# Performance work log

Measured on AMD Instinct MI355X. Metric: run time of the kernel, lower is better.

The kernel has to match this reference:

```python
import jax, jax.numpy as jnp
import numpy as np

EPS = 1e-8
BOX2D_IDX = jnp.array([0, 1, 3, 4, 6])  # x, y, dx, dy, yaw


def box2corners(box):
    # box: (..., 5) = (x, y, w, h, alpha) -> corners (..., 4, 2), CCW order
    x, y, w, h, a = (box[..., i] for i in range(5))
    tx = jnp.array([0.5, -0.5, -0.5, 0.5], box.dtype)
    ty = jnp.array([0.5, 0.5, -0.5, -0.5], box.dtype)
    x4 = tx * w[..., None]
    y4 = ty * h[..., None]
    c, s = jnp.cos(a)[..., None], jnp.sin(a)[..., None]
    rx = c * x4 - s * y4 + x[..., None]
    ry = s * x4 + c * y4 + y[..., None]
    return jnp.stack([rx, ry], axis=-1)


def edge_intersections(c1, c2):
    # all 4x4 edge-edge intersections of two quads -> pts (..., 16, 2), mask (..., 16)
    p1 = c1[..., :, None, :]
    p2 = jnp.roll(c1, -1, axis=-2)[..., :, None, :]
    q1 = c2[..., None, :, :]
    q2 = jnp.roll(c2, -1, axis=-2)[..., None, :, :]
    r = p2 - p1
    s = q2 - q1
    denom = r[..., 0] * s[..., 1] - r[..., 1] * s[..., 0]
    safe = jnp.where(jnp.abs(denom) < EPS, 1.0, denom)
    qp = q1 - p1
    t = (qp[..., 0] * s[..., 1] - qp[..., 1] * s[..., 0]) / safe
    u = (qp[..., 0] * r[..., 1] - qp[..., 1] * r[..., 0]) / safe
    mask = (jnp.abs(denom) > EPS) & (t > 0) & (t < 1) & (u > 0) & (u < 1)
    pts = jnp.where(mask[..., None], p1 + t[..., None] * r, 0.0)
    lead = pts.shape[:-3]
    return pts.reshape(lead + (16, 2)), mask.reshape(lead + (16,))


def points_in_box(pts, corners):
    # pts (..., K, 2) inside rotated quad given by corners (..., 4, 2) -> (..., K) bool
    a = corners[..., 0:1, :]
    ab = corners[..., 1:2, :] - a
    ad = corners[..., 3:4, :] - a
    ap = pts - a
    pab = jnp.sum(ap * ab, -1)
    pad = jnp.sum(ap * ad, -1)
    nab = jnp.sum(ab * ab, -1)
    nad = jnp.sum(ad * ad, -1)
    return (pab > 0) & (pab < nab) & (pad > 0) & (pad < nad)


def masked_polygon_area(verts, mask):
    # verts (..., 24, 2) candidate vertices, mask (..., 24) validity
    m = mask.astype(verts.dtype)
    num = jnp.maximum(jnp.sum(m, -1, keepdims=True), 1.0)
    mean = jnp.sum(verts * m[..., None], -2, keepdims=True) / num[..., None]
    d = verts - mean  # centered (shoelace is translation-invariant)
    ang = jnp.arctan2(d[..., 1], d[..., 0])
    # push invalid vertices to the end with stable tie-break
    ang = jnp.where(mask, ang, 1e6 + jnp.arange(24, dtype=ang.dtype))
    idx = jnp.argsort(ang, axis=-1)
    vs = jnp.take_along_axis(d, idx[..., None], axis=-2)
    ms = jnp.take_along_axis(mask, idx, axis=-1)
    v0 = vs[..., 0:1, :]
    vs = jnp.where(ms[..., None], vs, v0)  # collapse invalid onto first vertex
    nxt = jnp.roll(vs, -1, axis=-2)
    cross = vs[..., 0] * nxt[..., 1] - vs[..., 1] * nxt[..., 0]
    return 0.5 * jnp.abs(jnp.sum(cross, -1))


def rotated_iou_3d(b1, b2):
    # b1, b2: (..., 7) = (x, y, z, dx, dy, dz, yaw); elementwise-aligned IoU
    c1 = box2corners(b1[..., BOX2D_IDX])
    c2 = box2corners(b2[..., BOX2D_IDX])
    ipts, imask = edge_intersections(c1, c2)
    in1 = points_in_box(c1, c2)
    in2 = points_in_box(c2, c1)
    verts = jnp.concatenate([c1, c2, ipts], axis=-2)  # (..., 24, 2)
    mask = jnp.concatenate([in1, in2, imask], axis=-1)
    inter2d = masked_polygon_area(verts, mask)
    zmax = jnp.minimum(b1[..., 2] + 0.5 * b1[..., 5], b2[..., 2] + 0.5 * b2[..., 5])
    zmin = jnp.maximum(b1[..., 2] - 0.5 * b1[..., 5], b2[..., 2] - 0.5 * b2[..., 5])
    inter3d = inter2d * jnp.maximum(zmax - zmin, 0.0)
    v1 = b1[..., 3] * b1[..., 4] * b1[..., 5]
    v2 = b2[..., 3] * b2[..., 4] * b2[..., 5]
    return inter3d / (v1 + v2 - inter3d + EPS)


def setup_inputs() -> dict:
    key = jax.random.key(0)
    k1, k2, k3, k4, k5 = jax.random.split(key, 5)
    N = 1048576
    ctr = (jax.random.uniform(k1, (N, 3)) - 0.5) * 40.0
    dims = jax.random.uniform(k2, (N, 3)) * 2.0 + 0.5
    yaw = (jax.random.uniform(k3, (N, 1)) - 0.5) * (2.0 * np.pi)
    pred = jnp.concatenate([ctr, dims, yaw], axis=-1).astype(jnp.float32)
    noise = jax.random.normal(k4, (N, 7)) * jnp.array(
        [0.3, 0.3, 0.3, 0.2, 0.2, 0.2, 0.2], jnp.float32)
    target = pred + noise
    target = target.at[:, 3:6].set(jnp.maximum(target[:, 3:6], 0.1))
    weight = jax.random.uniform(k5, (N,), dtype=jnp.float32)
    return {"pred": pred, "target": target, "weight": weight}


def reference(pred, target, weight):
    # IoU3DLoss(with_yaw=True, reduction='mean', loss_weight=1.0)
    loss_weight = 1.0
    iou = rotated_iou_3d(pred[None, ...], target[None, ...])  # (1, N)
    iou_loss = (1.0 - iou) * weight
    return loss_weight * jnp.mean(iou_loss)
```

## Files before the change

### kernel.cpp

```cpp
#include <hip/hip_runtime.h>

#define EPS_F 1e-8f

__device__ __forceinline__ float fast_rcp(float x) {
    return __builtin_amdgcn_rcpf(x);
}

__global__ void zero_out_kernel(float* out) { out[0] = 0.f; }

__device__ __forceinline__ float edge_contrib(float ax, float ay,
                                              float bx, float by,
                                              float W, float H) {
    float dx = bx - ax, dy = by - ay;
    float sdx = (fabsf(dx) < 1e-20f) ? 1e-20f : dx;
    float sdy = (fabsf(dy) < 1e-20f) ? 1e-20f : dy;
    float rdx = fast_rcp(sdx);
    float rdy = fast_rcp(sdy);

    float tA = (-W - ax) * rdx;
    float tB = ( W - ax) * rdx;
    float ta = fmaxf(fminf(tA, tB), 0.f);
    float tb = fminf(fmaxf(tA, tB), 1.f);
    tb = fmaxf(ta, tb);

    float u0 = (-H - ay) * rdy;
    float u1 = ( H - ay) * rdy;
    float tm0 = fminf(u0, u1), tm1 = fmaxf(u0, u1);
    float t1 = fminf(fmaxf(tm0, ta), tb);
    float t2 = fminf(fmaxf(tm1, ta), tb);

    float x0 = fmaf(ta, dx, ax), y0 = fmaf(ta, dy, ay);
    float x1 = fmaf(t1, dx, ax), y1 = fmaf(t1, dy, ay);
    float x2 = fmaf(t2, dx, ax), y2 = fmaf(t2, dy, ay);
    float x3 = fmaf(tb, dx, ax), y3 = fmaf(tb, dy, ay);
    float h0 = fminf(fmaxf(y0, -H), H) + H;
    float h1 = fminf(fmaxf(y1, -H), H) + H;
    float h2 = fminf(fmaxf(y2, -H), H) + H;
    float h3 = fminf(fmaxf(y3, -H), H) + H;

    return (x1 - x0) * (h0 + h1) + (x2 - x1) * (h1 + h2) + (x3 - x2) * (h2 + h3);
}

#define EPT 2

__global__ __launch_bounds__(256) void iou3d_loss_kernel(
    const float* __restrict__ pred, const float* __restrict__ target,
    const float* __restrict__ weight, float* __restrict__ out,
    int N, float invN)
{
    int base = blockIdx.x * (256 * EPT) + threadIdx.x;
    float val = 0.f;

    #pragma unroll
    for (int e = 0; e < EPT; ++e) {
        int i = base + e * 256;
        if (i >= N) continue;

        float b1[7], b2[7];
        #pragma unroll
        for (int k = 0; k < 7; ++k) b1[k] = pred[(long)i * 7 + k];
        #pragma unroll
        for (int k = 0; k < 7; ++k) b2[k] = target[(long)i * 7 + k];
        float wgt = weight[i];

        float s1, c1, s2, c2;
        __sincosf(b1[6], &s1, &c1);
        __sincosf(b2[6], &s2, &c2);
        float cd = c1 * c2 + s1 * s2;
        float sd = c1 * s2 - s1 * c2;
        float dxc = b2[0] - b1[0], dyc = b2[1] - b1[1];
        float tx =  c1 * dxc + s1 * dyc;
        float ty = -s1 * dxc + c1 * dyc;
        float W = 0.5f * b1[3], H = 0.5f * b1[4];
        float w2 = 0.5f * b2[3], h2 = 0.5f * b2[4];

        float q0x = cd * ( w2) - sd * ( h2) + tx, q0y = sd * ( w2) + cd * ( h2) + ty;
        float q1x = cd * (-w2) - sd * ( h2) + tx, q1y = sd * (-w2) + cd * ( h2) + ty;
        float q2x = cd * (-w2) - sd * (-h2) + tx, q2y = sd * (-w2) + cd * (-h2) + ty;
        float q3x = cd * ( w2) - sd * (-h2) + tx, q3y = sd * ( w2) + cd * (-h2) + ty;

        float s  = edge_contrib(q0x, q0y, q1x, q1y, W, H)
                 + edge_contrib(q1x, q1y, q2x, q2y, W, H)
                 + edge_contrib(q2x, q2y, q3x, q3y, W, H)
                 + edge_contrib(q3x, q3y, q0x, q0y, W, H);
        float area = 0.5f * fabsf(s);

        float zmax = fminf(b1[2] + 0.5f * b1[5], b2[2] + 0.5f * b2[5]);
        float zmin = fmaxf(b1[2] - 0.5f * b1[5], b2[2] - 0.5f * b2[5]);
        float inter3d = area * fmaxf(zmax - zmin, 0.f);
        float v1 = b1[3] * b1[4] * b1[5];
        float v2 = b2[3] * b2[4] * b2[5];
        float iou = inter3d / (v1 + v2 - inter3d + EPS_F);
        val += (1.f - iou) * wgt * invN;
    }

    #pragma unroll
    for (int off = 32; off > 0; off >>= 1) val += __shfl_down(val, off, 64);
    __shared__ float wsum[4];
    int lane = threadIdx.x & 63, wid = threadIdx.x >> 6;
    if (lane == 0) wsum[wid] = val;
    __syncthreads();
    if (threadIdx.x == 0) {
        float ssum = wsum[0] + wsum[1] + wsum[2] + wsum[3];
        atomicAdd(out, ssum);
    }
}

extern "C" void kernel_launch(void* const* d_in, const int* in_sizes, int n_in,
                              void* d_out, int out_size, void* d_ws, size_t ws_size,
                              hipStream_t stream) {
    const float* pred   = (const float*)d_in[0];
    const float* target = (const float*)d_in[1];
    const float* weight = (const float*)d_in[2];
    float* out = (float*)d_out;
    int N = in_sizes[2];

    zero_out_kernel<<<1, 1, 0, stream>>>(out);
    int block = 256;
    int grid = (N + block * EPT - 1) / (block * EPT);
    iou3d_loss_kernel<<<grid, block, 0, stream>>>(pred, target, weight, out,
                                                  N, 1.f / (float)N);
}
```

Before: 114.0 us.

## Batch all global loads up front with four elements per thread

Each thread now handles four elements instead of two and issues every pred, target and weight load before starting any arithmetic, so more memory requests are in flight at once. Out-of-range lanes are clamped to index 0 and given zero weight, so the compute loop has no early continue. The IoU division is replaced by a hardware reciprocal multiply, and the launch bounds now request four waves per SIMD. The cost is higher register pressure from holding 60 loaded values, a grid half as large, and slightly lower precision in the IoU divide.

Result: faster. 101.1 us (-11.3%).

```diff
diff --git a/kernel.cpp b/kernel.cpp
--- a/kernel.cpp
+++ b/kernel.cpp
@@ -1,6 +1,7 @@
 #include <hip/hip_runtime.h>
 
 #define EPS_F 1e-8f
+#define EPT 4
 
 __device__ __forceinline__ float fast_rcp(float x) {
     return __builtin_amdgcn_rcpf(x);
@@ -41,38 +42,38 @@
     return (x1 - x0) * (h0 + h1) + (x2 - x1) * (h1 + h2) + (x3 - x2) * (h2 + h3);
 }
 
-#define EPT 2
-
-__global__ __launch_bounds__(256) void iou3d_loss_kernel(
+__global__ __launch_bounds__(256, 4) void iou3d_loss_kernel(
     const float* __restrict__ pred, const float* __restrict__ target,
     const float* __restrict__ weight, float* __restrict__ out,
     int N, float invN)
 {
     int base = blockIdx.x * (256 * EPT) + threadIdx.x;
-    float val = 0.f;
 
+    float b1[EPT][7], b2[EPT][7], wgt[EPT];
     #pragma unroll
     for (int e = 0; e < EPT; ++e) {
         int i = base + e * 256;
-        if (i >= N) continue;
+        int j = (i < N) ? i : 0;
+        #pragma unroll
+        for (int k = 0; k < 7; ++k) b1[e][k] = pred[(long)j * 7 + k];
+        #pragma unroll
+        for (int k = 0; k < 7; ++k) b2[e][k] = target[(long)j * 7 + k];
+        wgt[e] = (i < N) ? weight[j] : 0.f;
+    }
 
-        float b1[7], b2[7];
-        #pragma unroll
-        for (int k = 0; k < 7; ++k) b1[k] = pred[(long)i * 7 + k];
-        #pragma unroll
-        for (int k = 0; k < 7; ++k) b2[k] = target[(long)i * 7 + k];
-        float wgt = weight[i];
-
+    float val = 0.f;
+    #pragma unroll
+    for (int e = 0; e < EPT; ++e) {
         float s1, c1, s2, c2;
-        __sincosf(b1[6], &s1, &c1);
-        __sincosf(b2[6], &s2, &c2);
+        __sincosf(b1[e][6], &s1, &c1);
+        __sincosf(b2[e][6], &s2, &c2);
         float cd = c1 * c2 + s1 * s2;
         float sd = c1 * s2 - s1 * c2;
-        float dxc = b2[0] - b1[0], dyc = b2[1] - b1[1];
+        float dxc = b2[e][0] - b1[e][0], dyc = b2[e][1] - b1[e][1];
         float tx =  c1 * dxc + s1 * dyc;
         float ty = -s1 * dxc + c1 * dyc;
-        float W = 0.5f * b1[3], H = 0.5f * b1[4];
-        float w2 = 0.5f * b2[3], h2 = 0.5f * b2[4];
+        float W = 0.5f * b1[e][3], H = 0.5f * b1[e][4];
+        float w2 = 0.5f * b2[e][3], h2 = 0.5f * b2[e][4];
 
         float q0x = cd * ( w2) - sd * ( h2) + tx, q0y = sd * ( w2) + cd * ( h2) + ty;
         float q1x = cd * (-w2) - sd * ( h2) + tx, q1y = sd * (-w2) + cd * ( h2) + ty;
@@ -85,13 +86,13 @@
                  + edge_contrib(q3x, q3y, q0x, q0y, W, H);
         float area = 0.5f * fabsf(s);
 
-        float zmax = fminf(b1[2] + 0.5f * b1[5], b2[2] + 0.5f * b2[5]);
-        float zmin = fmaxf(b1[2] - 0.5f * b1[5], b2[2] - 0.5f * b2[5]);
+        float zmax = fminf(b1[e][2] + 0.5f * b1[e][5], b2[e][2] + 0.5f * b2[e][5]);
+        float zmin = fmaxf(b1[e][2] - 0.5f * b1[e][5], b2[e][2] - 0.5f * b2[e][5]);
         float inter3d = area * fmaxf(zmax - zmin, 0.f);
-        float v1 = b1[3] * b1[4] * b1[5];
-        float v2 = b2[3] * b2[4] * b2[5];
-        float iou = inter3d / (v1 + v2 - inter3d + EPS_F);
-        val += (1.f - iou) * wgt * invN;
+        float v1 = b1[e][3] * b1[e][4] * b1[e][5];
+        float v2 = b2[e][3] * b2[e][4] * b2[e][5];
+        float iou = inter3d * fast_rcp(v1 + v2 - inter3d + EPS_F);
+        val += (1.f - iou) * wgt[e] * invN;
     }
 
     #pragma unroll
```
